# Kernel tuning notes

Hardware: AMD Instinct MI355X
Metric: run time of the kernel (lower is better)

The kernel has to match this reference:

```python
import jax, jax.numpy as jnp
import numpy as np

N = 20000   # nodes
E = 200000  # edges
D = 32      # inp_dim == out_dim == emb_dim
R = 100     # num_rel
EPS = 1e-5  # BatchNorm1d default eps


def setup_inputs() -> dict:
    key = jax.random.key(0)
    ks = jax.random.split(key, 5)
    h = jax.random.normal(ks[0], (N, D), dtype=jnp.float32)
    # xavier_uniform-ish scale for [R, D, D] relation weights
    weight = jax.random.normal(ks[1], (R, D, D), dtype=jnp.float32) * (1.0 / np.sqrt(D))
    gamma = jnp.ones((D,), dtype=jnp.float32)
    beta = jnp.zeros((D,), dtype=jnp.float32)
    src = jax.random.randint(ks[2], (E,), 0, N, dtype=jnp.int32)
    dst = jax.random.randint(ks[3], (E,), 0, N, dtype=jnp.int32)
    etype = jax.random.randint(ks[4], (E,), 0, R, dtype=jnp.int32)
    return {"h": h, "weight": weight, "gamma": gamma, "beta": beta,
            "src": src, "dst": dst, "etype": etype}


def reference(h, weight, gamma, beta, src, dst, etype):
    # per-edge relation-weight gather: [E, D, D]
    w_e = weight[etype]
    # per-edge bmm (src feature row-vector @ relation matrix) + relu: [E, D]
    msg = jax.nn.relu(jnp.einsum('ed,edo->eo', h[src], w_e))
    # BatchNorm1d in training mode: batch stats over the edge dimension
    mu = jnp.mean(msg, axis=0)
    var = jnp.mean(jnp.square(msg - mu), axis=0)  # biased variance
    msg = (msg - mu) * jax.lax.rsqrt(var + EPS) * gamma + beta
    # segment-mean reduce of messages into destination nodes: [N, D]
    ssum = jax.ops.segment_sum(msg, dst, num_segments=N)
    cnt = jax.ops.segment_sum(jnp.ones((E,), msg.dtype), dst, num_segments=N)
    return ssum / jnp.maximum(cnt, 1.0)[:, None]
```

## Files before the change

### kernel.cpp

```cpp
#include <hip/hip_runtime.h>

#define D 32
#define EPS 1e-5f
#define TPB 256
#define NB 256
#define NMAX 20480

__global__ void histE_kernel(const int* __restrict__ etype, int E, int R, int chunk,
                             int* __restrict__ blockHistT)
{
    __shared__ int lh[1024];
    for (int i = threadIdx.x; i < R; i += TPB) lh[i] = 0;
    __syncthreads();
    const int lo = blockIdx.x * chunk, hi = min(E, lo + chunk);
    for (int e = lo + threadIdx.x; e < hi; e += TPB)
        atomicAdd(&lh[etype[e]], 1);
    __syncthreads();
    for (int r = threadIdx.x; r < R; r += TPB)
        blockHistT[r * NB + blockIdx.x] = lh[r];
}

__global__ void scanEa_kernel(int* __restrict__ blockHistT, int* __restrict__ relTot)
{
    __shared__ int buf[NB];
    int* p = blockHistT + blockIdx.x * NB;
    const int t = threadIdx.x;
    const int v = p[t];
    buf[t] = v;
    __syncthreads();
    int x = v;
    for (int off = 1; off < NB; off <<= 1) {
        const int y = (t >= off) ? buf[t - off] : 0;
        __syncthreads();
        x += y;
        buf[t] = x;
        __syncthreads();
    }
    p[t] = x - v;
    if (t == NB - 1) relTot[blockIdx.x] = x;
}

__global__ void scanEb_kernel(const int* __restrict__ relTot, int R,
                              int* __restrict__ rel_start,
                              int* __restrict__ task_rel, int* __restrict__ task_start,
                              int* __restrict__ n_tasks)
{
    __shared__ int s_tot[1024];
    __shared__ int s_start[1024];
    __shared__ int s_tbase[1024];
    for (int r = threadIdx.x; r < R; r += TPB) s_tot[r] = relTot[r];
    __syncthreads();
    if (threadIdx.x == 0) {
        int acc = 0, tb = 0;
        for (int r = 0; r < R; ++r) {
            s_start[r] = acc; s_tbase[r] = tb;
            acc += s_tot[r];
            tb  += (s_tot[r] + TPB - 1) / TPB;
        }
        rel_start[R] = acc;
        *n_tasks = tb;
    }
    __syncthreads();
    for (int r = threadIdx.x; r < R; r += TPB) {
        const int st = s_start[r];
        rel_start[r] = st;
        const int nb = (s_tot[r] + TPB - 1) / TPB;
        const int tb = s_tbase[r];
        for (int b = 0; b < nb; ++b) {
            task_rel[tb + b]   = r;
            task_start[tb + b] = st + b * TPB;
        }
    }
}

__global__ void scatterE_kernel(const int* __restrict__ src, const int* __restrict__ dst,
                                const int* __restrict__ etype, int E, int R, int chunk,
                                const int* __restrict__ blockHistT,
                                const int* __restrict__ rel_start,
                                int* __restrict__ ssrc, int* __restrict__ sdst,
                                int* __restrict__ nodeCnt)
{
    __shared__ int cur[1024];
    for (int r = threadIdx.x; r < R; r += TPB)
        cur[r] = rel_start[r] + blockHistT[r * NB + blockIdx.x];
    __syncthreads();
    const int lo = blockIdx.x * chunk, hi = min(E, lo + chunk);
    for (int e = lo + threadIdx.x; e < hi; e += TPB) {
        const int d = dst[e];
        const int p = atomicAdd(&cur[etype[e]], 1);
        ssrc[p] = src[e];
        sdst[p] = d;
        atomicAdd(&nodeCnt[d], 1);
    }
}

__global__ __launch_bounds__(1024)
void scanD_kernel(const int* __restrict__ nodeCnt, int N, int E,
                  int* __restrict__ node_start, int* __restrict__ curD)
{
    __shared__ int s_cnt[NMAX];
    __shared__ int s_part[1024];
    const int t = threadIdx.x;
    for (int i = t; i < N; i += 1024) s_cnt[i] = nodeCnt[i];
    __syncthreads();
    const int per = (N + 1023) / 1024;
    const int lo = min(t * per, N), hi = min(lo + per, N);
    int s = 0;
    for (int n = lo; n < hi; ++n) s += s_cnt[n];
    s_part[t] = s;
    __syncthreads();
    int x = s;
    for (int off = 1; off < 1024; off <<= 1) {
        const int y = (t >= off) ? s_part[t - off] : 0;
        __syncthreads();
        x += y;
        s_part[t] = x;
        __syncthreads();
    }
    int run = x - s;
    for (int n = lo; n < hi; ++n) { const int v = s_cnt[n]; s_cnt[n] = run; run += v; }
    __syncthreads();
    for (int i = t; i < N; i += 1024) {
        const int v = s_cnt[i];
        node_start[i] = v;
        curD[i] = v;
    }
    if (t == 1023) node_start[N] = E;
}

__global__ __launch_bounds__(TPB)
void rgcn_compute(const float* __restrict__ h, const float* __restrict__ W,
                  const int* __restrict__ rel_start,
                  const int* __restrict__ task_rel, const int* __restrict__ task_start,
                  const int* __restrict__ n_tasks_p,
                  const int* __restrict__ ssrc, const int* __restrict__ sdst,
                  int* __restrict__ curD, int* __restrict__ perm,
                  float* __restrict__ msg,
                  float* __restrict__ stat_sum, float* __restrict__ stat_sq)
{
    __shared__ float s_tile[TPB * 33];
    __shared__ int   s_src[TPB];
    __shared__ float s_aux[2 * TPB];

    const int task = blockIdx.x;
    if (task >= *n_tasks_p) return;
    const int r      = task_rel[task];
    const int start  = task_start[task];
    const int relEnd = rel_start[r + 1];
    const int nE     = min(TPB, relEnd - start);
    const int tid    = threadIdx.x;

    if (tid < nE) {
        s_src[tid] = ssrc[start + tid];
        const int p = atomicAdd(&curD[sdst[start + tid]], 1);
        perm[p] = start + tid;
    }
    __syncthreads();

    for (int i = tid; i < nE * 8; i += TPB) {
        const int row = i >> 3, seg = i & 7;
        const float4 v = *(const float4*)(h + (size_t)s_src[row] * D + seg * 4);
        float* p = &s_tile[row * 33 + seg * 4];
        p[0] = v.x; p[1] = v.y; p[2] = v.z; p[3] = v.w;
    }
    __syncthreads();

    const float* Wr = W + (size_t)__builtin_amdgcn_readfirstlane(r) * (D * D);

    float acc[D];
#pragma unroll
    for (int o = 0; o < D; ++o) acc[o] = 0.f;

    if (tid < nE) {
#pragma unroll 4
        for (int d = 0; d < D; ++d) {
            const float hd = s_tile[tid * 33 + d];
#pragma unroll
            for (int o = 0; o < D; ++o)
                acc[o] = fmaf(hd, Wr[d * D + o], acc[o]);
        }
#pragma unroll
        for (int o = 0; o < D; ++o) acc[o] = fmaxf(acc[o], 0.f);
    }
    __syncthreads();

    if (tid < nE) {
#pragma unroll
        for (int o = 0; o < D; ++o) s_tile[tid * 33 + o] = acc[o];
    }
    __syncthreads();

    float ps = 0.f, pq = 0.f;
    float* mbase = msg + (size_t)start * D;
    for (int i = tid; i < nE * D; i += TPB) {
        const int row = i >> 5, o = i & 31;
        const float v = s_tile[row * 33 + o];
        mbase[i] = v;
        ps += v; pq += v * v;
    }
    s_aux[tid]       = ps;
    s_aux[TPB + tid] = pq;
    __syncthreads();
    if (tid < D) {
        float ss = 0.f, sq = 0.f;
#pragma unroll
        for (int c = 0; c < TPB / D; ++c) {
            ss += s_aux[c * D + tid];
            sq += s_aux[TPB + c * D + tid];
        }
        atomicAdd(&stat_sum[tid], ss);
        atomicAdd(&stat_sq[tid],  sq);
    }
}

__global__ void reduce_kernel(const float* __restrict__ msg, const int* __restrict__ perm,
                              const int* __restrict__ node_start,
                              const float* __restrict__ stat_sum,
                              const float* __restrict__ stat_sq,
                              const float* __restrict__ gamma,
                              const float* __restrict__ beta,
                              float invE, float* __restrict__ out, int N)
{
    const int o = threadIdx.x & 31;
    const int n = blockIdx.x * 8 + (threadIdx.x >> 5);
    if (n >= N) return;
    const int j0 = node_start[n], j1 = node_start[n + 1];
    float s = 0.f;
    for (int j = j0; j < j1; ++j) {
        const int e = perm[j];
        s += msg[(size_t)e * D + o];
    }
    const float mu  = stat_sum[o] * invE;
    const float var = fmaxf(stat_sq[o] * invE - mu * mu, 0.f);
    const float is  = rsqrtf(var + EPS);
    const float sc  = gamma[o] * is;
    const float sh  = fmaf(-mu, sc, beta[o]);
    const float c   = (float)(j1 - j0);
    out[(size_t)n * D + o] = fmaf(s, sc, sh * c) / fmaxf(c, 1.0f);
}

extern "C" void kernel_launch(void* const* d_in, const int* in_sizes, int n_in,
                              void* d_out, int out_size, void* d_ws, size_t ws_size,
                              hipStream_t stream)
{
    const float* h     = (const float*)d_in[0];
    const float* W     = (const float*)d_in[1];
    const float* gamma = (const float*)d_in[2];
    const float* beta  = (const float*)d_in[3];
    const int*   src   = (const int*)d_in[4];
    const int*   dst   = (const int*)d_in[5];
    const int*   etype = (const int*)d_in[6];
    float* out = (float*)d_out;

    const int E = in_sizes[4];
    const int N = in_sizes[0] / D;
    const int R = in_sizes[1] / (D * D);
    const int T = R + (E + TPB - 1) / TPB;
    const int chunk = (E + NB - 1) / NB;

    int*   nodeCnt   = (int*)d_ws;
    float* stat_sum  = (float*)(nodeCnt + N);
    float* stat_sq   = stat_sum + D;
    int*   node_start= (int*)(stat_sq + D);
    int*   curD      = node_start + N + 1;
    int*   relTot    = curD + N;
    int*   rel_start = relTot + R;
    int*   n_tasks   = rel_start + R + 1;
    int*   blockHistT= n_tasks + 1;
    int*   task_rel  = blockHistT + R * NB;
    int*   task_start= task_rel + T;
    int*   ssrc      = task_start + T;
    int*   sdst      = ssrc + E;
    int*   perm      = sdst + E;
    float* msg       = (float*)(perm + E);

    hipMemsetAsync(d_ws, 0, sizeof(int) * (size_t)(N + 2 * D), stream);

    histE_kernel<<<NB, TPB, 0, stream>>>(etype, E, R, chunk, blockHistT);
    scanEa_kernel<<<R, TPB, 0, stream>>>(blockHistT, relTot);
    scanEb_kernel<<<1, TPB, 0, stream>>>(relTot, R, rel_start,
                                         task_rel, task_start, n_tasks);
    scatterE_kernel<<<NB, TPB, 0, stream>>>(src, dst, etype, E, R, chunk,
                                            blockHistT, rel_start, ssrc, sdst, nodeCnt);
    scanD_kernel<<<1, 1024, 0, stream>>>(nodeCnt, N, E, node_start, curD);
    rgcn_compute<<<T, TPB, 0, stream>>>(h, W, rel_start, task_rel, task_start,
                                        n_tasks, ssrc, sdst, curD, perm,
                                        msg, stat_sum, stat_sq);
    reduce_kernel<<<(N + 7) / 8, TPB, 0, stream>>>(msg, perm, node_start,
                                                   stat_sum, stat_sq, gamma, beta,
                                                   1.0f / (float)E, out, N);
}
```

Before: 159.1 us.

## Merge the scan kernels into one launch and batch perm loads via shuffles in reduce

The node-degree histogram moves into the edge-type histogram kernel, and the two edge-type scan kernels plus the node scan become a single one-block kernel that scans the flattened relation-by-block histogram and the node counts. This cuts the launch count from seven kernels to five and removes the separate rel_start add in scatter. The reduce kernel now has each warp load 32 perm indices at once and broadcast them with shuffles, rather than every lane loading each index in turn. The cost is a larger serial single-block scan over 25600 entries, with a matching increase in shared memory use.

```diff
diff --git a/kernel.cpp b/kernel.cpp
--- a/kernel.cpp
+++ b/kernel.cpp
@@ -4,128 +4,132 @@
 #define EPS 1e-5f
 #define TPB 256
 #define NB 256
-#define NMAX 20480
-
-__global__ void histE_kernel(const int* __restrict__ etype, int E, int R, int chunk,
-                             int* __restrict__ blockHistT)
+#define RNB_MAX 25600
+#define SCAN_T 1024
+
+__global__ void histE_kernel(const int* __restrict__ etype, const int* __restrict__ dst,
+                             int E, int R, int chunk,
+                             int* __restrict__ blockHistT,
+                             int* __restrict__ nodeCnt)
 {
     __shared__ int lh[1024];
     for (int i = threadIdx.x; i < R; i += TPB) lh[i] = 0;
     __syncthreads();
     const int lo = blockIdx.x * chunk, hi = min(E, lo + chunk);
-    for (int e = lo + threadIdx.x; e < hi; e += TPB)
+    for (int e = lo + threadIdx.x; e < hi; e += TPB) {
         atomicAdd(&lh[etype[e]], 1);
+        atomicAdd(&nodeCnt[dst[e]], 1);
+    }
     __syncthreads();
     for (int r = threadIdx.x; r < R; r += TPB)
         blockHistT[r * NB + blockIdx.x] = lh[r];
 }
 
-__global__ void scanEa_kernel(int* __restrict__ blockHistT, int* __restrict__ relTot)
-{
-    __shared__ int buf[NB];
-    int* p = blockHistT + blockIdx.x * NB;
+__global__ __launch_bounds__(SCAN_T)
+void scanAll_kernel(int* __restrict__ blockHistT, int R,
+                    const int* __restrict__ nodeCnt, int N, int E,
+                    int* __restrict__ rel_start,
+                    int* __restrict__ task_rel, int* __restrict__ task_start,
+                    int* __restrict__ n_tasks,
+                    int* __restrict__ node_start, int* __restrict__ curD)
+{
+    __shared__ int s_buf[RNB_MAX];
+    __shared__ int s_part[SCAN_T];
+    __shared__ int s_tbase[1024];
     const int t = threadIdx.x;
-    const int v = p[t];
-    buf[t] = v;
-    __syncthreads();
-    int x = v;
-    for (int off = 1; off < NB; off <<= 1) {
-        const int y = (t >= off) ? buf[t - off] : 0;
+
+    const int M = R * NB;
+    for (int i = t; i < M; i += SCAN_T) s_buf[i] = blockHistT[i];
+    __syncthreads();
+    {
+        const int per = (M + SCAN_T - 1) / SCAN_T;
+        const int lo = min(t * per, M), hi = min(lo + per, M);
+        int s = 0;
+        for (int i = lo; i < hi; ++i) s += s_buf[i];
+        s_part[t] = s;
         __syncthreads();
-        x += y;
-        buf[t] = x;
+        int x = s;
+        for (int off = 1; off < SCAN_T; off <<= 1) {
+            const int y = (t >= off) ? s_part[t - off] : 0;
+            __syncthreads();
+            x += y;
+            s_part[t] = x;
+            __syncthreads();
+        }
+        int run = x - s;
+        for (int i = lo; i < hi; ++i) { const int v = s_buf[i]; s_buf[i] = run; run += v; }
+    }
+    __syncthreads();
+    for (int i = t; i < M; i += SCAN_T) blockHistT[i] = s_buf[i];
+    for (int r = t; r < R; r += SCAN_T) rel_start[r] = s_buf[r * NB];
+    if (t == 0) rel_start[R] = E;
+    if (t == 0) {
+        int tb = 0;
+        for (int r = 0; r < R; ++r) {
+            const int st  = s_buf[r * NB];
+            const int en  = (r + 1 < R) ? s_buf[(r + 1) * NB] : E;
+            s_tbase[r] = tb;
+            tb += (en - st + TPB - 1) / TPB;
+        }
+        *n_tasks = tb;
+    }
+    __syncthreads();
+    if (t < R) {
+        const int st = s_buf[t * NB];
+        const int en = (t + 1 < R) ? s_buf[(t + 1) * NB] : E;
+        const int nb = (en - st + TPB - 1) / TPB;
+        const int tb = s_tbase[t];
+        for (int b = 0; b < nb; ++b) {
+            task_rel[tb + b]   = t;
+            task_start[tb + b] = st + b * TPB;
+        }
+    }
+    __syncthreads();
+
+    for (int i = t; i < N; i += SCAN_T) s_buf[i] = nodeCnt[i];
+    __syncthreads();
+    {
+        const int per = (N + SCAN_T - 1) / SCAN_T;
+        const int lo = min(t * per, N), hi = min(lo + per, N);
+        int s = 0;
+        for (int i = lo; i < hi; ++i) s += s_buf[i];
+        s_part[t] = s;
         __syncthreads();
-    }
-    p[t] = x - v;
-    if (t == NB - 1) relTot[blockIdx.x] = x;
-}
-
-__global__ void scanEb_kernel(const int* __restrict__ relTot, int R,
-                              int* __restrict__ rel_start,
-                              int* __restrict__ task_rel, int* __restrict__ task_start,
-                              int* __restrict__ n_tasks)
-{
-    __shared__ int s_tot[1024];
-    __shared__ int s_start[1024];
-    __shared__ int s_tbase[1024];
-    for (int r = threadIdx.x; r < R; r += TPB) s_tot[r] = relTot[r];
-    __syncthreads();
-    if (threadIdx.x == 0) {
-        int acc = 0, tb = 0;
-        for (int r = 0; r < R; ++r) {
-            s_start[r] = acc; s_tbase[r] = tb;
-            acc += s_tot[r];
-            tb  += (s_tot[r] + TPB - 1) / TPB;
-        }
-        rel_start[R] = acc;
-        *n_tasks = tb;
-    }
-    __syncthreads();
-    for (int r = threadIdx.x; r < R; r += TPB) {
-        const int st = s_start[r];
-        rel_start[r] = st;
-        const int nb = (s_tot[r] + TPB - 1) / TPB;
-        const int tb = s_tbase[r];
-        for (int b = 0; b < nb; ++b) {
-            task_rel[tb + b]   = r;
-            task_start[tb + b] = st + b * TPB;
-        }
-    }
+        int x = s;
+        for (int off = 1; off < SCAN_T; off <<= 1) {
+            const int y = (t >= off) ? s_part[t - off] : 0;
+            __syncthreads();
+            x += y;
+            s_part[t] = x;
+            __syncthreads();
+        }
+        int run = x - s;
+        for (int i = lo; i < hi; ++i) { const int v = s_buf[i]; s_buf[i] = run; run += v; }
+    }
+    __syncthreads();
+    for (int i = t; i < N; i += SCAN_T) {
+        const int v = s_buf[i];
+        node_start[i] = v;
+        curD[i] = v;
+    }
+    if (t == 0) node_start[N] = E;
 }
 
 __global__ void scatterE_kernel(const int* __restrict__ src, const int* __restrict__ dst,
                                 const int* __restrict__ etype, int E, int R, int chunk,
                                 const int* __restrict__ blockHistT,
-                                const int* __restrict__ rel_start,
-                                int* __restrict__ ssrc, int* __restrict__ sdst,
-                                int* __restrict__ nodeCnt)
+                                int* __restrict__ ssrc, int* __restrict__ sdst)
 {
     __shared__ int cur[1024];
     for (int r = threadIdx.x; r < R; r += TPB)
-        cur[r] = rel_start[r] + blockHistT[r * NB + blockIdx.x];
+        cur[r] = blockHistT[r * NB + blockIdx.x];
     __syncthreads();
     const int lo = blockIdx.x * chunk, hi = min(E, lo + chunk);
     for (int e = lo + threadIdx.x; e < hi; e += TPB) {
-        const int d = dst[e];
         const int p = atomicAdd(&cur[etype[e]], 1);
         ssrc[p] = src[e];
-        sdst[p] = d;
-        atomicAdd(&nodeCnt[d], 1);
-    }
-}
-
-__global__ __launch_bounds__(1024)
-void scanD_kernel(const int* __restrict__ nodeCnt, int N, int E,
-                  int* __restrict__ node_start, int* __restrict__ curD)
-{
-    __shared__ int s_cnt[NMAX];
-    __shared__ int s_part[1024];
-    const int t = threadIdx.x;
-    for (int i = t; i < N; i += 1024) s_cnt[i] = nodeCnt[i];
-    __syncthreads();
-    const int per = (N + 1023) / 1024;
-    const int lo = min(t * per, N), hi = min(lo + per, N);
-    int s = 0;
-    for (int n = lo; n < hi; ++n) s += s_cnt[n];
-    s_part[t] = s;
-    __syncthreads();
-    int x = s;
-    for (int off = 1; off < 1024; off <<= 1) {
-        const int y = (t >= off) ? s_part[t - off] : 0;
-        __syncthreads();
-        x += y;
-        s_part[t] = x;
-        __syncthreads();
-    }
-    int run = x - s;
-    for (int n = lo; n < hi; ++n) { const int v = s_cnt[n]; s_cnt[n] = run; run += v; }
-    __syncthreads();
-    for (int i = t; i < N; i += 1024) {
-        const int v = s_cnt[i];
-        node_start[i] = v;
-        curD[i] = v;
-    }
-    if (t == 1023) node_start[N] = E;
+        sdst[p] = dst[e];
+    }
 }
 
 __global__ __launch_bounds__(TPB)
@@ -226,9 +230,14 @@
     if (n >= N) return;
     const int j0 = node_start[n], j1 = node_start[n + 1];
     float s = 0.f;
-    for (int j = j0; j < j1; ++j) {
-        const int e = perm[j];
-        s += msg[(size_t)e * D + o];
+    for (int base = j0; base < j1; base += 32) {
+        const int cnt = min(32, j1 - base);
+        const int myj = (o < cnt) ? perm[base + o] : 0;
+#pragma unroll 8
+        for (int k = 0; k < cnt; ++k) {
+            const int e = __shfl(myj, k, 32);
+            s += msg[(size_t)e * D + o];
+        }
     }
     const float mu  = stat_sum[o] * invE;
     const float var = fmaxf(stat_sq[o] * invE - mu * mu, 0.f);
@@ -263,8 +272,7 @@
     float* stat_sq   = stat_sum + D;
     int*   node_start= (int*)(stat_sq + D);
     int*   curD      = node_start + N + 1;
-    int*   relTot    = curD + N;
-    int*   rel_start = relTot + R;
+    int*   rel_start = curD + N;
     int*   n_tasks   = rel_start + R + 1;
     int*   blockHistT= n_tasks + 1;
     int*   task_rel  = blockHistT + R * NB;
@@ -276,13 +284,12 @@
 
     hipMemsetAsync(d_ws, 0, sizeof(int) * (size_t)(N + 2 * D), stream);
 
-    histE_kernel<<<NB, TPB, 0, stream>>>(etype, E, R, chunk, blockHistT);
-    scanEa_kernel<<<R, TPB, 0, stream>>>(blockHistT, relTot);
-    scanEb_kernel<<<1, TPB, 0, stream>>>(relTot, R, rel_start,
-                                         task_rel, task_start, n_tasks);
+    histE_kernel<<<NB, TPB, 0, stream>>>(etype, dst, E, R, chunk, blockHistT, nodeCnt);
+    scanAll_kernel<<<1, SCAN_T, 0, stream>>>(blockHistT, R, nodeCnt, N, E,
+                                             rel_start, task_rel, task_start, n_tasks,
+                                             node_start, curD);
     scatterE_kernel<<<NB, TPB, 0, stream>>>(src, dst, etype, E, R, chunk,
-                                            blockHistT, rel_start, ssrc, sdst, nodeCnt);
-    scanD_kernel<<<1, 1024, 0, stream>>>(nodeCnt, N, E, node_start, curD);
+                                            blockHistT, ssrc, sdst);
     rgcn_compute<<<T, TPB, 0, stream>>>(h, W, rel_start, task_rel, task_start,
                                         n_tasks, ssrc, sdst, curD, perm,
                                         msg, stat_sum, stat_sq);
```

Result: slower. 162.8 us (+2.3%).
